# Kernel optimization log

Measured on AMD Instinct MI355X. Metric: run time of the kernel, lower is better.

Reference implementation:

```python
import jax, jax.numpy as jnp
import numpy as np

Bsz, T, D = 2, 2048, 1024
H_ATTN, HD, WIN = 16, 64, 128
H_SSM, DI, N, DCONV, DTR = 8, 2048, 16, 4, 64
P = DI // H_SSM
DT_MIN, DT_MAX = 1e-4, 1.0
EPS = 1e-6


def setup_inputs() -> dict:
    key = jax.random.key(0)
    ks = jax.random.split(key, 16)
    def g(i, shp, s=0.02):
        return jax.random.normal(ks[i], shp, jnp.float32) * s
    TOT = 2 * DI + DTR + 2 * H_SSM * N
    # dt_bias = inverse_softplus(dt) with dt log-uniform in [dt_min, dt_max]
    dt0 = jnp.exp(jax.random.uniform(ks[14], (H_SSM,), jnp.float32) * (np.log(DT_MAX) - np.log(DT_MIN)) + np.log(DT_MIN))
    dt_bias = dt0 + jnp.log(-jnp.expm1(-dt0))
    return dict(
        x=jax.random.normal(ks[0], (Bsz, T, D), jnp.float32),
        norm1_w=jnp.ones((D,), jnp.float32),
        norm2_w=jnp.ones((D,), jnp.float32),
        Win=g(1, (TOT, D)),
        Wdt=g(2, (H_SSM, DTR)),
        conv_w=g(3, (DI, DCONV), 0.2),
        conv_b=jnp.zeros((DI,), jnp.float32),
        A_log=jnp.log(jnp.broadcast_to(jnp.arange(1, N + 1, dtype=jnp.float32), (H_SSM, N))),
        Dskip=jnp.ones((H_SSM, P), jnp.float32),
        dt_bias=dt_bias,
        ssd_norm_w=jnp.ones((DI,), jnp.float32),
        Wout_ssd=g(4, (D, DI)),
        Wres=g(5, (DI, D)),
        Wq=g(6, (D, D)), Wk=g(7, (D, D)), Wv=g(8, (D, D)), Wo=g(9, (D, D)),
    )


def _rms(x, w):
    return x * jax.lax.rsqrt(jnp.mean(x * x, -1, keepdims=True) + EPS) * w


def _silu(x):
    return x * jax.nn.sigmoid(x)


def _dwconv(x, w, b):
    # causal depthwise conv1d: x [B,T,C], w [C,K], left-pad K-1
    K = w.shape[1]
    xp = jnp.pad(x, ((0, 0), (K - 1, 0), (0, 0)))
    y = sum(xp[:, k:k + x.shape[1], :] * w[:, k] for k in range(K))
    return y + b


def _rope(q, k):
    # q,k: [B,H,T,HD]
    inv = 1.0 / (10000.0 ** (jnp.arange(0, HD, 2, dtype=jnp.float32) / HD))
    t = jnp.arange(q.shape[2], dtype=jnp.float32)
    f = jnp.concatenate([t[:, None] * inv, t[:, None] * inv], -1)  # [T,HD]
    cos, sin = jnp.cos(f), jnp.sin(f)
    def rot(x):
        h = x.shape[-1] // 2
        return jnp.concatenate([-x[..., h:], x[..., :h]], -1)
    return q * cos + rot(q) * sin, k * cos + rot(k) * sin


def _ssd_branch(u, Win, Wdt, conv_w, conv_b, A_log, Dskip, dt_bias, ssd_norm_w, Wout_ssd, Wres):
    B = u.shape[0]
    proj = u @ Win.T  # [B,T,4416]
    xin = proj[..., :DI]
    z = proj[..., DI:2 * DI]
    dtl = proj[..., 2 * DI:2 * DI + DTR]
    o = 2 * DI + DTR
    Bm = proj[..., o:o + H_SSM * N].reshape(B, T, H_SSM, N)
    Cm = proj[..., o + H_SSM * N:].reshape(B, T, H_SSM, N)
    xc = _silu(_dwconv(xin, conv_w, conv_b))
    dt = jnp.clip(jax.nn.softplus(dtl @ Wdt.T + dt_bias), DT_MIN, DT_MAX)  # [B,T,H]
    A = -jnp.exp(A_log)  # [H,N]
    xh = xc.reshape(B, T, H_SSM, P)
    dA = jnp.exp(dt[..., None] * A)  # [B,T,H,N]
    dtB = dt[..., None] * Bm        # [B,T,H,N]

    def step(h, inp):
        dA_t, dtB_t, x_t, C_t = inp
        h = h * dA_t[:, :, None, :] + x_t[..., None] * dtB_t[:, :, None, :]
        y = jnp.einsum('bhpn,bhn->bhp', h, C_t)
        return h, y

    h0 = jnp.zeros((B, H_SSM, P, N), u.dtype)
    _, ys = jax.lax.scan(step, h0, (
        dA.transpose(1, 0, 2, 3), dtB.transpose(1, 0, 2, 3),
        xh.transpose(1, 0, 2, 3), Cm.transpose(1, 0, 2, 3)))
    y = ys.transpose(1, 0, 2, 3) + Dskip * xh  # [B,T,H,P]
    y = y.reshape(B, T, DI) + u @ Wres.T       # residual_proj(d_model->d_inner)
    y = _rms(y * _silu(z), ssd_norm_w)         # fused gated RMSNorm
    return y @ Wout_ssd.T


def _attn(u, Wq, Wk, Wv, Wo):
    B = u.shape[0]
    q = (u @ Wq.T).reshape(B, T, H_ATTN, HD).transpose(0, 2, 1, 3)
    k = (u @ Wk.T).reshape(B, T, H_ATTN, HD).transpose(0, 2, 1, 3)
    v = (u @ Wv.T).reshape(B, T, H_ATTN, HD).transpose(0, 2, 1, 3)
    q, k = _rope(q, k)
    s = jnp.einsum('bhtd,bhsd->bhts', q, k) / np.sqrt(HD).astype(np.float32)
    rel = jnp.arange(T)[:, None] - jnp.arange(T)[None, :]
    allowed = (rel >= 0) & (rel < WIN)  # causal sliding window
    s = jnp.where(allowed, s, jnp.float32(-1e30))
    p = jax.nn.softmax(s, axis=-1)
    y = jnp.einsum('bhts,bhsd->bhtd', p, v)
    return y.transpose(0, 2, 1, 3).reshape(B, T, D) @ Wo.T


def reference(x, norm1_w, norm2_w, Win, Wdt, conv_w, conv_b, A_log, Dskip, dt_bias,
              ssd_norm_w, Wout_ssd, Wres, Wq, Wk, Wv, Wo):
    h = x + _ssd_branch(_rms(x, norm1_w), Win, Wdt, conv_w, conv_b, A_log, Dskip,
                        dt_bias, ssd_norm_w, Wout_ssd, Wres)
    return h + _attn(_rms(h, norm2_w), Wq, Wk, Wv, Wo)
```

## Files before the change

kernel.cpp:

```cpp
#include <hip/hip_runtime.h>
#include <stdint.h>

typedef unsigned short u16;
typedef unsigned int u32;
typedef __attribute__((ext_vector_type(8))) short short8;
typedef __attribute__((ext_vector_type(4))) unsigned short ushort4v;
typedef __attribute__((ext_vector_type(4))) float f32x4;

#define Bsz 2
#define Tn 2048
#define Dm 1024
#define H_ATTN 16
#define HDx 64
#define WINx 128
#define H_SSM 8
#define DIx 2048
#define Nst 16
#define DTRx 64
#define Px 256
#define TOTx 4416
#define TOT2 6464
#define RESOFF 4416
#define OFFC (2*DIx+DTRx+H_SSM*Nst)
#define BT (Bsz*Tn)
#define NCH 32
#define LCH 64

__device__ __forceinline__ float b2f(u16 u){ u32 x = ((u32)u)<<16; float f; __builtin_memcpy(&f,&x,4); return f; }
__device__ __forceinline__ u16 f2b(float f){ u32 x; __builtin_memcpy(&x,&f,4); u32 r = x + 0x7fffu + ((x>>16)&1u); return (u16)(r>>16); }

__device__ __forceinline__ float block_sum256(float v){
  #pragma unroll
  for (int o=32;o;o>>=1) v += __shfl_xor(v,o,64);
  __shared__ float sb[4];
  int wid = threadIdx.x>>6;
  if ((threadIdx.x&63)==0) sb[wid]=v;
  __syncthreads();
  v = sb[0]+sb[1]+sb[2]+sb[3];
  __syncthreads();
  return v;
}

__device__ __forceinline__ void gload_lds16(const void* g, void* l){
  __builtin_amdgcn_global_load_lds((const __attribute__((address_space(1))) void*)g,
                                   (__attribute__((address_space(3))) void*)l, 16, 0, 0);
}

struct CvtArgs { const float* s[7]; u16* d[7]; int n[7]; };
__global__ __launch_bounds__(256) void k_cvt_all(CvtArgs a, int total4){
  int i = blockIdx.x*256 + threadIdx.x;
  if (i >= total4) return;
  int e = i*4;
  #pragma unroll
  for (int j=0;j<7;j++){
    if (e < a.n[j]){
      float4 v = *(const float4*)(a.s[j]+e);
      u16* d = a.d[j]+e;
      d[0]=f2b(v.x); d[1]=f2b(v.y); d[2]=f2b(v.z); d[3]=f2b(v.w);
      return;
    }
    e -= a.n[j];
  }
}

__global__ __launch_bounds__(256) void k_rms1024(const float* __restrict__ src, const float* __restrict__ w,
                                                 u16* __restrict__ dst){
  int row = blockIdx.x, tid = threadIdx.x;
  const float* s = src + (size_t)row*1024;
  float v[4]; float ss=0.f;
  #pragma unroll
  for (int i=0;i<4;i++){ v[i] = s[tid + i*256]; ss += v[i]*v[i]; }
  ss = block_sum256(ss);
  float sc = rsqrtf(ss*(1.0f/1024.0f) + 1e-6f);
  u16* d = dst + (size_t)row*1024;
  #pragma unroll
  for (int i=0;i<4;i++){ int c = tid+i*256; d[c] = f2b(v[i]*sc*w[c]); }
}

#define BKq 64

__global__ __launch_bounds__(512,1)
void k_gemm256(const u16* __restrict__ A, const u16* __restrict__ W,
               u16* __restrict__ C16, int M, int N, int K, int gxx){
  __shared__ u16 lds[2][4][128*64];
  int tid = threadIdx.x, lane = tid&63, wid = tid>>6;
  int bid = blockIdx.x;
  int xcd = bid&7, r = bid>>3;
  int halfg = gxx>>1;
  int row0 = (xcd>>1)<<2, col0 = (xcd&1)*halfg;
  int bx = col0 + (r>>2), by = row0 + (r&3);
  int bm = by*256, bn = bx*256;
  int wr = wid>>2, wcn = wid&3;
  int fr = lane&15, fq = lane>>4;
  f32x4 acc[2][2][4][2];
  #pragma unroll
  for (int a=0;a<2;a++)
    #pragma unroll
    for (int b=0;b<2;b++)
      #pragma unroll
      for (int c=0;c<4;c++)
        #pragma unroll
        for (int d=0;d<2;d++)
          #pragma unroll
          for (int rr=0;rr<4;rr++) acc[a][b][c][d][rr]=0.f;

  auto stageHalf = [&](int b, int q, int tt){
    int k0 = tt*BKq;
    #pragma unroll
    for (int i=0;i<2;i++){
      int idx = i*512 + tid;
      int row = idx>>3, c8 = idx&7;
      const u16* src; int gr;
      if (q < 2){ gr = bm + q*128 + row;     if (gr > M-1) gr = M-1; src = A; }
      else      { gr = bn + (q-2)*128 + row; if (gr > N-1) gr = N-1; src = W; }
      gload_lds16(src + (size_t)gr*K + k0 + ((c8 ^ (row&7)))*8, &lds[b][q][(size_t)idx*8]);
    }
  };
  auto loadA = [&](const u16* aP, short8 (&af)[2][4]){
    #pragma unroll
    for (int kk=0;kk<2;kk++)
      #pragma unroll
      for (int mi=0;mi<4;mi++){
        int row = wr*64 + mi*16 + fr;
        af[kk][mi] = *(const short8*)(aP + row*64 + ((kk*4+fq) ^ (row&7))*8);
      }
  };
  auto loadB = [&](const u16* bP, short8 (&bf)[2][2]){
    #pragma unroll
    for (int kk=0;kk<2;kk++)
      #pragma unroll
      for (int ni=0;ni<2;ni++){
        int row = wcn*32 + ni*16 + fr;
        bf[kk][ni] = *(const short8*)(bP + row*64 + ((kk*4+fq) ^ (row&7))*8);
      }
  };

  int NT = K/BKq;
  stageHalf(0,0,0); stageHalf(0,2,0); stageHalf(0,3,0); stageHalf(0,1,0);

  short8 af[2][4], bf0[2][2], bf1[2][2];
  for (int t=0;t<NT;t++){
    int cb = t&1, nb = cb^1;
    int tn = (t+1 < NT) ? t+1 : t;
    const u16* A0 = &lds[cb][0][0];
    const u16* A1 = &lds[cb][1][0];
    const u16* B0 = &lds[cb][2][0];
    const u16* B1 = &lds[cb][3][0];
    stageHalf(nb,0,tn);
    asm volatile("s_waitcnt vmcnt(6)" ::: "memory");
    __builtin_amdgcn_sched_barrier(0);
    __builtin_amdgcn_s_barrier();
    loadA(A0, af); loadB(B0, bf0);
    asm volatile("s_waitcnt lgkmcnt(0)" ::: "memory");
    __builtin_amdgcn_sched_barrier(0);
    __builtin_amdgcn_s_setprio(1);
    #pragma unroll
    for (int kk=0;kk<2;kk++)
      #pragma unroll
      for (int mi=0;mi<4;mi++)
        #pragma unroll
        for (int ni=0;ni<2;ni++)
          acc[0][0][mi][ni] = __builtin_amdgcn_mfma_f32_16x16x32_bf16(af[kk][mi], bf0[kk][ni], acc[0][0][mi][ni], 0,0,0);
    __builtin_amdgcn_s_setprio(0);
    __builtin_amdgcn_s_barrier();
    stageHalf(nb,2,tn);
    asm volatile("s_waitcnt vmcnt(6)" ::: "memory");
    __builtin_amdgcn_sched_barrier(0);
    __builtin_amdgcn_s_barrier();
    loadB(B1, bf1);
    asm volatile("s_waitcnt lgkmcnt(0)" ::: "memory");
    __builtin_amdgcn_sched_barrier(0);
    __builtin_amdgcn_s_setprio(1);
    #pragma unroll
    for (int kk=0;kk<2;kk++)
      #pragma unroll
      for (int mi=0;mi<4;mi++)
        #pragma unroll
        for (int ni=0;ni<2;ni++)
          acc[0][1][mi][ni] = __builtin_amdgcn_mfma_f32_16x16x32_bf16(af[kk][mi], bf1[kk][ni], acc[0][1][mi][ni], 0,0,0);
    __builtin_amdgcn_s_setprio(0);
    __builtin_amdgcn_s_barrier();
    stageHalf(nb,3,tn);
    asm volatile("s_waitcnt vmcnt(6)" ::: "memory");
    __builtin_amdgcn_sched_barrier(0);
    __builtin_amdgcn_s_barrier();
    loadA(A1, af);
    asm volatile("s_waitcnt lgkmcnt(0)" ::: "memory");
    __builtin_amdgcn_sched_barrier(0);
    __builtin_amdgcn_s_setprio(1);
    #pragma unroll
    for (int kk=0;kk<2;kk++)
      #pragma unroll
      for (int mi=0;mi<4;mi++)
        #pragma unroll
        for (int ni=0;ni<2;ni++)
          acc[1][1][mi][ni] = __builtin_amdgcn_mfma_f32_16x16x32_bf16(af[kk][mi], bf1[kk][ni], acc[1][1][mi][ni], 0,0,0);
    __builtin_amdgcn_s_setprio(0);
    __builtin_amdgcn_s_barrier();
    stageHalf(nb,1,tn);
    asm volatile("s_waitcnt vmcnt(6)" ::: "memory");
    __builtin_amdgcn_sched_barrier(0);
    __builtin_amdgcn_s_barrier();
    __builtin_amdgcn_s_setprio(1);
    #pragma unroll
    for (int kk=0;kk<2;kk++)
      #pragma unroll
      for (int mi=0;mi<4;mi++)
        #pragma unroll
        for (int ni=0;ni<2;ni++)
          acc[1][0][mi][ni] = __builtin_amdgcn_mfma_f32_16x16x32_bf16(af[kk][mi], bf0[kk][ni], acc[1][0][mi][ni], 0,0,0);
    __builtin_amdgcn_s_setprio(0);
    __builtin_amdgcn_s_barrier();
  }
  #pragma unroll
  for (int mh=0;mh<2;mh++)
    #pragma unroll
    for (int nh=0;nh<2;nh++)
      #pragma unroll
      for (int mi=0;mi<4;mi++)
        #pragma unroll
        for (int ni=0;ni<2;ni++){
          int row0o = bm + mh*128 + wr*64 + mi*16 + fq*4;
          int col  = bn + nh*128 + wcn*32 + ni*16 + fr;
          if (col < N){
            #pragma unroll
            for (int rr=0;rr<4;rr++)
              C16[(size_t)(row0o+rr)*N + col] = f2b(acc[mh][nh][mi][ni][rr]);
          }
        }
}

template<int NWC>
__global__ __launch_bounds__(256, (NWC==2?2:3))
void k_gemm(const u16* __restrict__ A, const u16* __restrict__ W,
            float* __restrict__ C, u16* __restrict__ C16, const float* __restrict__ ADD,
            int M, int N, int K, int gx, int mode){
  constexpr int BN    = 64*NWC;
  constexpr int ROWS  = 128 + BN;
  constexpr int NLOADS= ROWS/32;
  constexpr int MFRAG = (NWC==2)?4:2;
  __shared__ u16 lds[2][ROWS*64];
  int tid = threadIdx.x, lane = tid&63, wid = tid>>6;
  int nwg = gridDim.x;
  int cpx = nwg>>3;
  int bid = blockIdx.x;
  int swz = (bid&7)*cpx + (bid>>3);
  int fourgx = gx<<2;
  int super = swz / fourgx;
  int r     = swz % fourgx;
  int bx = r >> 2;
  int by = (super<<2) + (r&3);
  int bm = by*128, bn = bx*BN;
  int wc = (NWC==2) ? (wid&1) : 0;
  int wr = (NWC==2) ? (wid>>1) : wid;
  int fr = lane&15, fq = lane>>4;
  int s7 = fr&7;
  f32x4 acc[MFRAG][4];
  #pragma unroll
  for (int mi=0;mi<MFRAG;mi++)
    #pragma unroll
    for (int ni=0;ni<4;ni++)
      #pragma unroll
      for (int rr=0;rr<4;rr++) acc[mi][ni][rr]=0.f;

  auto stage = [&](int buf, int t){
    int k0 = t*BKq;
    #pragma unroll
    for (int i=0;i<NLOADS;i++){
      int chunk = i*256 + tid;
      int row = chunk>>3, c8 = chunk&7;
      const u16* src;
      if (row < 128){ int ra = bm + row; if (ra > M-1) ra = M-1; src = A + (size_t)ra*K; }
      else          { int rb = bn + row-128; if (rb > N-1) rb = N-1; src = W + (size_t)rb*K; }
      gload_lds16(src + k0 + ((c8 ^ (row&7)))*8, &lds[buf][(size_t)chunk*8]);
    }
  };

  int NT = K/BKq;
  stage(0, 0);
  stage(1, 1);
  for (int t=0;t<NT;t++){
    int cur = t&1;
    if (t+1 < NT){
      if constexpr (NWC==2) asm volatile("s_waitcnt vmcnt(8)" ::: "memory");
      else                  asm volatile("s_waitcnt vmcnt(6)" ::: "memory");
    } else {
      asm volatile("s_waitcnt vmcnt(0)" ::: "memory");
    }
    __builtin_amdgcn_sched_barrier(0);
    __builtin_amdgcn_s_barrier();
    #pragma unroll
    for (int kk=0;kk<2;kk++){
      short8 bf4[4], af4[MFRAG];
      int slotb = ((kk*4 + fq) ^ s7)*8;
      #pragma unroll
      for (int ni=0;ni<4;ni++)
        bf4[ni] = *(const short8*)(&lds[cur][(128 + wc*64 + ni*16 + fr)*64 + slotb]);
      #pragma unroll
      for (int mi=0;mi<MFRAG;mi++)
        af4[mi] = *(const short8*)(&lds[cur][(wr*(MFRAG*16) + mi*16 + fr)*64 + slotb]);
      #pragma unroll
      for (int mi=0;mi<MFRAG;mi++)
        #pragma unroll
        for (int ni=0;ni<4;ni++)
          acc[mi][ni] = __builtin_amdgcn_mfma_f32_16x16x32_bf16(af4[mi], bf4[ni], acc[mi][ni], 0,0,0);
    }
    asm volatile("s_waitcnt lgkmcnt(0)" ::: "memory");
    __builtin_amdgcn_sched_barrier(0);
    __builtin_amdgcn_s_barrier();
    if (t+2 < NT) stage(cur, t+2);
  }
  #pragma unroll
  for (int mi=0;mi<MFRAG;mi++){
    int row0 = bm + wr*(MFRAG*16) + mi*16 + fq*4;
    #pragma unroll
    for (int ni=0;ni<4;ni++){
      int col = bn + wc*64 + ni*16 + fr;
      if (col < N){
        #pragma unroll
        for (int rr=0;rr<4;rr++){
          size_t idx = (size_t)(row0+rr)*N + col;
          float v = acc[mi][ni][rr];
          if (mode == 0)      C[idx] = v;
          else if (mode == 2) C16[idx] = f2b(v);
          else                C[idx] = ADD[idx] + v;
        }
      }
    }
  }
}

__global__ __launch_bounds__(256) void k_dtprep(const u16* __restrict__ proj, const float* __restrict__ Wdt,
      const float* __restrict__ dt_bias, const float* __restrict__ A_log,
      float* __restrict__ dtA, float* __restrict__ dtB){
  int idx = blockIdx.x*256 + threadIdx.x;
  int h = idx & 7; int bt = idx >> 3;
  const u16* dtl  = proj + (size_t)bt*TOT2 + 2*DIx;
  const float* wrow = Wdt + h*64;
  float v = dt_bias[h];
  #pragma unroll
  for (int i8=0;i8<8;i8++){
    short8 dv = *(const short8*)(dtl + i8*8);
    #pragma unroll
    for (int e=0;e<8;e++) v += b2f((u16)dv[e])*wrow[i8*8+e];
  }
  float sp = (v > 20.0f) ? v : log1pf(expf(v));
  float dt = fminf(fmaxf(sp, 1e-4f), 1.0f);
  const u16* bm = proj + (size_t)bt*TOT2 + 2*DIx + DTRx + h*16;
  short8 b0 = *(const short8*)(bm);
  short8 b1 = *(const short8*)(bm+8);
  #pragma unroll
  for (int n=0;n<16;n++){
    float Av = -expf(A_log[h*16+n]);
    float bv = (n<8) ? b2f((u16)b0[n]) : b2f((u16)b1[n-8]);
    dtA[(size_t)idx*16+n] = dt*Av;
    dtB[(size_t)idx*16+n] = dt*bv;
  }
}

__global__ __launch_bounds__(256) void k_scan1(const float* __restrict__ dtA, const float* __restrict__ dtB,
    const u16* __restrict__ proj, const float* __restrict__ cw, const float* __restrict__ cb,
    float* __restrict__ expS, u16* __restrict__ y, float* __restrict__ LS){
  __shared__ float sA[1024], sS[1024], sB[1024], sC[1024];
  int bx = blockIdx.x;
  int c = bx & 31, h = (bx>>5)&7, b = bx>>8;
  int tid = threadIdx.x;
  size_t t0 = (size_t)b*Tn + c*64;
  int j = tid>>2, n0 = (tid&3)*4;
  {
    size_t ga = (t0 + j)*128 + h*16 + n0;
    float4 va = *(const float4*)(dtA + ga);
    float4 vb = *(const float4*)(dtB + ga);
    ushort4v vc = *(const ushort4v*)(proj + (t0 + j)*TOT2 + OFFC + h*16 + n0);
    *(float4*)(&sA[j*16+n0]) = va;
    *(float4*)(&sB[j*16+n0]) = vb;
    sC[j*16+n0+0] = b2f(vc[0]); sC[j*16+n0+1] = b2f(vc[1]);
    sC[j*16+n0+2] = b2f(vc[2]); sC[j*16+n0+3] = b2f(vc[3]);
  }
  __syncthreads();
  if (tid < 16){
    float cum = 0.f;
    for (int jj=0;jj<64;jj++){ cum += sA[jj*16+tid]; sS[jj*16+tid] = cum; }
  }
  __syncthreads();
  {
    float e[4], s4[4];
    #pragma unroll
    for (int i=0;i<4;i++){ e[i] = expf(sA[j*16+n0+i]); s4[i] = expf(sS[j*16+n0+i]); }
    #pragma unroll
    for (int i=0;i<4;i++){ sA[j*16+n0+i] = e[i]; sS[j*16+n0+i] = s4[i]; }
    float4 ev; ev.x=s4[0]; ev.y=s4[1]; ev.z=s4[2]; ev.w=s4[3];
    *(float4*)(expS + (t0+j)*128 + h*16 + n0) = ev;
  }
  __syncthreads();
  float st[16];
  #pragma unroll
  for (int n=0;n<16;n++) st[n]=0.f;
  int ch = h*Px + tid;
  const u16* pxin = proj + t0*TOT2 + ch;
  const u16* pres = proj + t0*TOT2 + RESOFF + ch;
  float w0=cw[ch*4+0], w1=cw[ch*4+1], w2=cw[ch*4+2], w3=cw[ch*4+3];
  float bcv = cb[ch];
  float x3=0.f, x2=0.f, x1=0.f;
  if (c > 0){
    x3 = b2f(pxin[-(ptrdiff_t)3*TOT2]);
    x2 = b2f(pxin[-(ptrdiff_t)2*TOT2]);
    x1 = b2f(pxin[-(ptrdiff_t)TOT2]);
  }
  u16* yp = y + t0*DIx + ch;
  for (int jj=0;jj<64;jj++){
    float x0 = b2f(pxin[(size_t)jj*TOT2]);
    float cv = bcv + x3*w0 + x2*w1 + x1*w2 + x0*w3;
    float x = cv / (1.0f + expf(-cv));
    x3=x2; x2=x1; x1=x0;
    float acc = b2f(pres[(size_t)jj*TOT2]);
    #pragma unroll
    for (int n=0;n<16;n++){ st[n] = st[n]*sA[jj*16+n] + x*sB[jj*16+n]; acc += st[n]*sC[jj*16+n]; }
    yp[(size_t)jj*DIx] = f2b(acc);
  }
  float* ls = LS + ((((size_t)b*8+h)*NCH + c)*Px + tid)*16;
  #pragma unroll
  for (int n=0;n<16;n++) ls[n] = st[n];
}

__global__ __launch_bounds__(256) void k_scan2(const float* __restrict__ expS, const float* __restrict__ LS,
                                               float* __restrict__ H0){
  int bh = blockIdx.x; int b = bh>>3, h = bh&7;
  int tid = threadIdx.x;
  __shared__ float dl[16];
  float Hs[16];
  #pragma unroll
  for (int n=0;n<16;n++) Hs[n]=0.f;
  for (int c=0;c<NCH;c++){
    if (tid<16) dl[tid] = expS[((size_t)b*Tn + c*64 + 63)*128 + h*16 + tid];
    __syncthreads();
    size_t base = ((((size_t)b*8+h)*NCH + c)*Px + tid)*16;
    #pragma unroll
    for (int n=0;n<16;n++){ H0[base+n] = Hs[n]; Hs[n] = Hs[n]*dl[n] + LS[base+n]; }
    __syncthreads();
  }
}

__global__ __launch_bounds__(256) void k_scan3(const u16* __restrict__ proj, const float* __restrict__ expS,
    const float* __restrict__ H0, const float* __restrict__ cw, const float* __restrict__ cb,
    const float* __restrict__ Dskip, u16* __restrict__ y){
  __shared__ float ce[1024];
  int bx = blockIdx.x; int c = bx&31, h=(bx>>5)&7, b=bx>>8;
  int tid = threadIdx.x;
  size_t t0 = (size_t)b*Tn + c*64;
  int j = tid>>2, n0=(tid&3)*4;
  {
    ushort4v cv = *(const ushort4v*)(proj + (t0+j)*TOT2 + OFFC + h*16 + n0);
    float4 evv = *(const float4*)(expS + (t0+j)*128 + h*16 + n0);
    ce[j*16+n0+0] = b2f(cv[0])*evv.x; ce[j*16+n0+1] = b2f(cv[1])*evv.y;
    ce[j*16+n0+2] = b2f(cv[2])*evv.z; ce[j*16+n0+3] = b2f(cv[3])*evv.w;
  }
  __syncthreads();
  float h0[16];
  size_t base = ((((size_t)b*8+h)*NCH + c)*Px + tid)*16;
  #pragma unroll
  for (int n=0;n<16;n++) h0[n] = H0[base+n];
  int ch = h*Px + tid;
  float dsk = Dskip[ch];
  const u16* pxin = proj + t0*TOT2 + ch;
  float w0=cw[ch*4+0], w1=cw[ch*4+1], w2=cw[ch*4+2], w3=cw[ch*4+3];
  float bcv = cb[ch];
  float x3=0.f, x2=0.f, x1=0.f;
  if (c > 0){
    x3 = b2f(pxin[-(ptrdiff_t)3*TOT2]);
    x2 = b2f(pxin[-(ptrdiff_t)2*TOT2]);
    x1 = b2f(pxin[-(ptrdiff_t)TOT2]);
  }
  u16* yp = y + t0*DIx + ch;
  for (int jj=0;jj<64;jj++){
    float x0 = b2f(pxin[(size_t)jj*TOT2]);
    float cv = bcv + x3*w0 + x2*w1 + x1*w2 + x0*w3;
    float x = cv / (1.0f + expf(-cv));
    x3=x2; x2=x1; x1=x0;
    float f = 0.f;
    #pragma unroll
    for (int n=0;n<16;n++) f += ce[jj*16+n]*h0[n];
    size_t yi = (size_t)jj*DIx;
    yp[yi] = f2b(b2f(yp[yi]) + f + dsk*x);
  }
}

__global__ __launch_bounds__(256) void k_gatedrms(const u16* __restrict__ y, const u16* __restrict__ proj,
     const float* __restrict__ w, u16* __restrict__ yn){
  int row = blockIdx.x, tid = threadIdx.x;
  const u16* yr = y + (size_t)row*DIx;
  const u16* zr = proj + (size_t)row*TOT2 + DIx;
  float v[8]; float ss=0.f;
  #pragma unroll
  for (int i=0;i<8;i++){
    int cidx = tid + i*256;
    float z = b2f(zr[cidx]);
    float g = b2f(yr[cidx]) * (z / (1.0f + expf(-z)));
    v[i]=g; ss += g*g;
  }
  ss = block_sum256(ss);
  float sc = rsqrtf(ss*(1.0f/2048.0f) + 1e-6f);
  u16* d = yn + (size_t)row*DIx;
  #pragma unroll
  for (int i=0;i<8;i++){ int cidx=tid+i*256; d[cidx] = f2b(v[i]*sc*w[cidx]); }
}

__global__ __launch_bounds__(256) void k_addrms(const float* __restrict__ x, const float* __restrict__ sout,
     const float* __restrict__ w, float* __restrict__ hbuf, u16* __restrict__ u2){
  int row=blockIdx.x, tid=threadIdx.x;
  float v[4]; float ss=0.f;
  #pragma unroll
  for (int i=0;i<4;i++){
    int cidx = tid + i*256;
    size_t idx = (size_t)row*1024 + cidx;
    float hv = x[idx] + sout[idx];
    hbuf[idx]=hv; v[i]=hv; ss+=hv*hv;
  }
  ss = block_sum256(ss);
  float sc = rsqrtf(ss*(1.0f/1024.0f)+1e-6f);
  #pragma unroll
  for (int i=0;i<4;i++){ int cidx=tid+i*256; u2[(size_t)row*1024+cidx] = f2b(v[i]*sc*w[cidx]); }
}

__global__ __launch_bounds__(256) void k_rope(const u16* __restrict__ qkvb,
    u16* __restrict__ qr, u16* __restrict__ kr, u16* __restrict__ vr){
  int idx = blockIdx.x*256 + threadIdx.x;
  int d = idx & 63;
  int h = (idx>>6) & 15;
  int t = (idx>>10) & 2047;
  int b = idx >> 21;
  int col = idx & 1023;
  size_t base = (size_t)(idx>>10)*3072;
  int dh = d & 31;
  float ang = (float)t * exp2f(-(float)dh * (13.287712379549449f/32.0f));
  float cs = cosf(ang), sn = sinf(ang);
  int part = (d<32) ? 32 : -32;
  float q = b2f(qkvb[base + col]),        qp = b2f(qkvb[base + col + part]);
  float k = b2f(qkvb[base + 1024 + col]), kp = b2f(qkvb[base + 1024 + col + part]);
  float vv = b2f(qkvb[base + 2048 + col]);
  float rq = (d<32)? -qp : qp;
  float rk = (d<32)? -kp : kp;
  size_t dst = (((size_t)b*H_ATTN + h)*Tn + t)*64 + d;
  qr[dst] = f2b(q*cs + rq*sn);
  kr[dst] = f2b(k*cs + rk*sn);
  vr[dst] = f2b(vv);
}

#define QT 64
#define KSPAN 192
__device__ __forceinline__ u32 swz128a(int row, int b){
  return (u32)((row*128 + b) ^ ((((row&7)^((row>>3)&7)))<<4));
}
__device__ __forceinline__ u32 swz384a(int row, int b){
  return (u32)((row*384 + b) ^ ((((row&7)^((row>>3)&7)))<<4));
}

__global__ __launch_bounds__(256) void k_attn_mfma(const u16* __restrict__ qr, const u16* __restrict__ kr,
    const u16* __restrict__ vr, u16* __restrict__ ya){
  __shared__ u16 bufK[KSPAN*64];
  __shared__ u16 bufV[64*KSPAN];
  int tid = threadIdx.x, lane = tid&63, wid = tid>>6;
  int fr = lane&15, fq = lane>>4;
  int blk = blockIdx.x;
  int qt = blk & 31, bh = blk >> 5;
  int t0 = qt*QT;
  size_t rowbase = (size_t)bh*Tn;
  char* cK = (char*)bufK;
  char* cV = (char*)bufV;

  #pragma unroll
  for (int it=0; it<6; ++it){
    int chunk = it*256 + tid;
    int row = chunk>>3, c8 = chunk&7;
    int sg = t0 - 128 + row;
    if (sg >= 0){
      short8 v = *(const short8*)(kr + (rowbase+sg)*64 + c8*8);
      *(short8*)(cK + swz128a(row, c8*16)) = v;
    }
  }
  #pragma unroll
  for (int it=0; it<6; ++it){
    int idx = it*256 + tid;
    int s = idx>>3, c8 = idx&7, d0 = c8*8;
    int sg = t0 - 128 + s;
    short8 v;
    if (sg >= 0) v = *(const short8*)(vr + (rowbase+sg)*64 + d0);
    else         v = short8{0,0,0,0,0,0,0,0};
    #pragma unroll
    for (int e=0;e<8;e++)
      *(u16*)(cV + swz384a(d0+e, s*2)) = (u16)v[e];
  }
  __syncthreads();

  f32x4 acc[12];
  #pragma unroll
  for (int j=0;j<12;j++)
    #pragma unroll
    for (int r=0;r<4;r++) acc[j][r]=0.f;
  #pragma unroll
  for (int kk=0;kk<2;kk++){
    short8 aq = *(const short8*)(qr + (rowbase + t0 + wid*16 + fr)*64 + kk*32 + fq*8);
    #pragma unroll
    for (int j=0;j<12;j++){
      short8 bk = *(const short8*)(cK + swz128a(j*16+fr, kk*64 + fq*16));
      acc[j] = __builtin_amdgcn_mfma_f32_16x16x32_bf16(aq, bk, acc[j], 0,0,0);
    }
  }

  float p[12][4];
  int cb = lane&15;
  #pragma unroll
  for (int r=0;r<4;r++){
    int rq = wid*16 + (lane>>4)*4 + r;
    float m = -3.0e38f;
    #pragma unroll
    for (int j=0;j<12;j++){
      int c = j*16 + cb;
      bool allowed = (c > rq) && (c <= rq+128) && (c >= 128 - t0);
      float v = allowed ? acc[j][r]*0.125f : -3.0e38f;
      p[j][r] = v;
      m = fmaxf(m, v);
    }
    #pragma unroll
    for (int o=1;o<16;o<<=1) m = fmaxf(m, __shfl_xor(m, o, 64));
    float sum = 0.f;
    #pragma unroll
    for (int j=0;j<12;j++){ float e = __expf(p[j][r]-m); p[j][r]=e; sum += e; }
    #pragma unroll
    for (int o=1;o<16;o<<=1) sum += __shfl_xor(sum, o, 64);
    float inv = 1.0f/sum;
    #pragma unroll
    for (int j=0;j<12;j++) p[j][r] *= inv;
  }
  __syncthreads();

  #pragma unroll
  for (int r=0;r<4;r++){
    int rq = wid*16 + (lane>>4)*4 + r;
    #pragma unroll
    for (int j=0;j<12;j++){
      *(u16*)(cK + swz384a(rq, (j*16+cb)*2)) = f2b(p[j][r]);
    }
  }
  __syncthreads();

  f32x4 acc2[4];
  #pragma unroll
  for (int f=0;f<4;f++)
    #pragma unroll
    for (int r=0;r<4;r++) acc2[f][r]=0.f;
  #pragma unroll
  for (int kk=0;kk<6;kk++){
    short8 ap = *(const short8*)(cK + swz384a(wid*16 + fr, kk*64 + fq*16));
    #pragma unroll
    for (int f=0;f<4;f++){
      short8 bv = *(const short8*)(cV + swz384a(f*16+fr, kk*64 + fq*16));
      acc2[f] = __builtin_amdgcn_mfma_f32_16x16x32_bf16(ap, bv, acc2[f], 0,0,0);
    }
  }
  int b = bh >> 4, h = bh & 15;
  #pragma unroll
  for (int f=0;f<4;f++){
    int d = f*16 + cb;
    #pragma unroll
    for (int r=0;r<4;r++){
      int q = t0 + wid*16 + (lane>>4)*4 + r;
      ya[((size_t)b*Tn + q)*Dm + h*64 + d] = f2b(acc2[f][r]);
    }
  }
}

extern "C" void kernel_launch(void* const* d_in, const int* in_sizes, int n_in,
                              void* d_out, int out_size, void* d_ws, size_t ws_size,
                              hipStream_t stream) {
  const float* x        = (const float*)d_in[0];
  const float* norm1_w  = (const float*)d_in[1];
  const float* norm2_w  = (const float*)d_in[2];
  const float* Win      = (const float*)d_in[3];
  const float* Wdt      = (const float*)d_in[4];
  const float* conv_w   = (const float*)d_in[5];
  const float* conv_b   = (const float*)d_in[6];
  const float* A_log    = (const float*)d_in[7];
  const float* Dskip    = (const float*)d_in[8];
  const float* dt_bias  = (const float*)d_in[9];
  const float* ssd_norm = (const float*)d_in[10];
  const float* Wout_ssd = (const float*)d_in[11];
  const float* Wres     = (const float*)d_in[12];
  const float* Wq       = (const float*)d_in[13];
  const float* Wk       = (const float*)d_in[14];
  const float* Wv       = (const float*)d_in[15];
  const float* Wo       = (const float*)d_in[16];

  char* ws = (char*)d_ws;
  size_t off = 0;
  auto alloc = [&](size_t bytes){ size_t r = off; off += (bytes + 255) & ~(size_t)255; return r; };

  size_t o_WinB  = alloc((size_t)TOTx*Dm*2);
  size_t o_WresB = alloc((size_t)DIx*Dm*2);
  size_t o_WoutB = alloc((size_t)Dm*DIx*2);
  size_t o_WqB   = alloc((size_t)Dm*Dm*2);
  size_t o_WkB   = alloc((size_t)Dm*Dm*2);
  size_t o_WvB   = alloc((size_t)Dm*Dm*2);
  size_t o_WoB   = alloc((size_t)Dm*Dm*2);
  size_t o_u1    = alloc((size_t)BT*Dm*2);
  size_t o_proj  = alloc((size_t)BT*TOT2*2);
  size_t o_sout  = alloc((size_t)BT*Dm*4);
  size_t o_dtA   = alloc((size_t)BT*H_SSM*Nst*4);
  size_t o_dtB   = alloc((size_t)BT*H_SSM*Nst*4);
  size_t o_expS  = alloc((size_t)BT*H_SSM*Nst*4);
  size_t o_LS    = alloc((size_t)Bsz*H_SSM*NCH*Px*Nst*4);
  size_t o_H0    = alloc((size_t)Bsz*H_SSM*NCH*Px*Nst*4);
  size_t o_y     = alloc((size_t)BT*DIx*2);
  size_t o_yn    = alloc((size_t)BT*DIx*2);
  size_t o_hb    = alloc((size_t)BT*Dm*4);
  size_t o_qr    = alloc((size_t)Bsz*H_ATTN*Tn*HDx*2);
  size_t o_kr    = alloc((size_t)Bsz*H_ATTN*Tn*HDx*2);

  u16* WinB  = (u16*)(ws + o_WinB);
  u16* WoutB = (u16*)(ws + o_WoutB);
  u16* WqB   = (u16*)(ws + o_WqB);
  u16* u1    = (u16*)(ws + o_u1);
  u16* projb = (u16*)(ws + o_proj);
  float* dtA  = (float*)(ws + o_dtA);
  float* dtB  = (float*)(ws + o_dtB);
  float* expS = (float*)(ws + o_expS);
  float* LS   = (float*)(ws + o_LS);
  float* H0   = (float*)(ws + o_H0);
  u16*   ybuf16 = (u16*)(ws + o_y);
  u16*   yn   = (u16*)(ws + o_yn);
  float* hb   = (float*)(ws + o_hb);
  float* sout = (float*)(ws + o_sout);
  u16* qkvb = (u16*)(ws + o_proj);
  u16* qr = (u16*)(ws + o_qr);
  u16* kr = (u16*)(ws + o_kr);
  u16* vr = u1;
  u16* yatt = (u16*)(ws + o_y);

  {
    CvtArgs a;
    a.s[0]=Win;  a.d[0]=WinB;  a.n[0]=TOTx*Dm;
    a.s[1]=Wres; a.d[1]=(u16*)(ws + o_WresB); a.n[1]=DIx*Dm;
    a.s[2]=Wout_ssd; a.d[2]=WoutB; a.n[2]=Dm*DIx;
    a.s[3]=Wq; a.d[3]=WqB; a.n[3]=Dm*Dm;
    a.s[4]=Wk; a.d[4]=(u16*)(ws + o_WkB); a.n[4]=Dm*Dm;
    a.s[5]=Wv; a.d[5]=(u16*)(ws + o_WvB); a.n[5]=Dm*Dm;
    a.s[6]=Wo; a.d[6]=(u16*)(ws + o_WoB); a.n[6]=Dm*Dm;
    int total4 = (a.n[0]+a.n[1]+a.n[2]+a.n[3]+a.n[4]+a.n[5]+a.n[6])/4;
    k_cvt_all<<<dim3((total4+255)/256), dim3(256), 0, stream>>>(a, total4);
  }

  k_rms1024<<<dim3(BT), dim3(256), 0, stream>>>(x, norm1_w, u1);
  k_gemm256<<<dim3(16*26), dim3(512), 0, stream>>>(u1, WinB, projb, BT, TOT2, Dm, 26);
  k_dtprep<<<dim3(BT*H_SSM/256), dim3(256), 0, stream>>>(projb, Wdt, dt_bias, A_log, dtA, dtB);
  k_scan1<<<dim3(Bsz*H_SSM*NCH), dim3(256), 0, stream>>>(dtA, dtB, projb, conv_w, conv_b, expS, ybuf16, LS);
  k_scan2<<<dim3(Bsz*H_SSM), dim3(256), 0, stream>>>(expS, LS, H0);
  k_scan3<<<dim3(Bsz*H_SSM*NCH), dim3(256), 0, stream>>>(projb, expS, H0, conv_w, conv_b, Dskip, ybuf16);
  k_gatedrms<<<dim3(BT), dim3(256), 0, stream>>>(ybuf16, projb, ssd_norm, yn);
  k_gemm<1><<<dim3(16*32), dim3(256), 0, stream>>>(yn, WoutB, sout, nullptr, nullptr, BT, Dm, DIx, 16, 0);
  k_addrms<<<dim3(BT), dim3(256), 0, stream>>>(x, sout, norm2_w, hb, (u16*)(ws + o_yn));
  u16* u2p = (u16*)(ws + o_yn);
  k_gemm<1><<<dim3(48*32), dim3(256), 0, stream>>>(u2p, WqB, nullptr, qkvb, nullptr, BT, 3*Dm, Dm, 48, 2);
  k_rope<<<dim3(BT*Dm/256), dim3(256), 0, stream>>>(qkvb, qr, kr, vr);
  k_attn_mfma<<<dim3(Bsz*H_ATTN*(Tn/QT)), dim3(256), 0, stream>>>(qr, kr, vr, yatt);
  k_gemm<1><<<dim3(16*32), dim3(256), 0, stream>>>(yatt, (u16*)(ws + o_WoB), (float*)d_out, nullptr, hb, BT, Dm, Dm, 16, 3);
  (void)in_sizes; (void)n_in; (void)out_size; (void)ws_size;
}
```

Baseline: 337.0 us.

## Collapse four-phase GEMM pipeline into one staged tile per iteration

Replaces the four-quadrant interleaved prefetch/compute schedule, which had a barrier and LDS wait per quadrant, with a simpler loop. Each iteration issues all four global→LDS stages for the next tile, waits for the current tile, loads all A/B fragments from LDS, then runs all four quadrant MFMA blocks back to back. This cuts barriers per k-step from eight to two. In exchange it holds more fragment registers at once (af0 and af1), which may raise register pressure and lower occupancy, and it loses the fine-grained overlap of LDS reads with MFMA.

```diff
diff --git a/kernel.cpp b/kernel.cpp
--- a/kernel.cpp
+++ b/kernel.cpp
@@ -136,80 +136,58 @@
   };
 
   int NT = K/BKq;
-  stageHalf(0,0,0); stageHalf(0,2,0); stageHalf(0,3,0); stageHalf(0,1,0);
-
-  short8 af[2][4], bf0[2][2], bf1[2][2];
+  stageHalf(0,0,0); stageHalf(0,1,0); stageHalf(0,2,0); stageHalf(0,3,0);
+
   for (int t=0;t<NT;t++){
     int cb = t&1, nb = cb^1;
-    int tn = (t+1 < NT) ? t+1 : t;
-    const u16* A0 = &lds[cb][0][0];
-    const u16* A1 = &lds[cb][1][0];
-    const u16* B0 = &lds[cb][2][0];
-    const u16* B1 = &lds[cb][3][0];
-    stageHalf(nb,0,tn);
-    asm volatile("s_waitcnt vmcnt(6)" ::: "memory");
+    if (t+1 < NT){
+      stageHalf(nb,0,t+1); stageHalf(nb,1,t+1); stageHalf(nb,2,t+1); stageHalf(nb,3,t+1);
+      asm volatile("s_waitcnt vmcnt(8)" ::: "memory");
+    } else {
+      asm volatile("s_waitcnt vmcnt(0)" ::: "memory");
+    }
     __builtin_amdgcn_sched_barrier(0);
     __builtin_amdgcn_s_barrier();
-    loadA(A0, af); loadB(B0, bf0);
-    asm volatile("s_waitcnt lgkmcnt(0)" ::: "memory");
     __builtin_amdgcn_sched_barrier(0);
-    __builtin_amdgcn_s_setprio(1);
-    #pragma unroll
-    for (int kk=0;kk<2;kk++)
-      #pragma unroll
-      for (int mi=0;mi<4;mi++)
+    {
+      const u16* A0 = &lds[cb][0][0];
+      const u16* A1 = &lds[cb][1][0];
+      const u16* B0 = &lds[cb][2][0];
+      const u16* B1 = &lds[cb][3][0];
+      short8 af0[2][4], af1[2][4], bf0[2][2], bf1[2][2];
+      loadA(A0, af0); loadB(B0, bf0); loadB(B1, bf1); loadA(A1, af1);
+      __builtin_amdgcn_s_setprio(1);
+      #pragma unroll
+      for (int kk=0;kk<2;kk++)
         #pragma unroll
-        for (int ni=0;ni<2;ni++)
-          acc[0][0][mi][ni] = __builtin_amdgcn_mfma_f32_16x16x32_bf16(af[kk][mi], bf0[kk][ni], acc[0][0][mi][ni], 0,0,0);
-    __builtin_amdgcn_s_setprio(0);
-    __builtin_amdgcn_s_barrier();
-    stageHalf(nb,2,tn);
-    asm volatile("s_waitcnt vmcnt(6)" ::: "memory");
+        for (int mi=0;mi<4;mi++)
+          #pragma unroll
+          for (int ni=0;ni<2;ni++)
+            acc[0][0][mi][ni] = __builtin_amdgcn_mfma_f32_16x16x32_bf16(af0[kk][mi], bf0[kk][ni], acc[0][0][mi][ni], 0,0,0);
+      #pragma unroll
+      for (int kk=0;kk<2;kk++)
+        #pragma unroll
+        for (int mi=0;mi<4;mi++)
+          #pragma unroll
+          for (int ni=0;ni<2;ni++)
+            acc[0][1][mi][ni] = __builtin_amdgcn_mfma_f32_16x16x32_bf16(af0[kk][mi], bf1[kk][ni], acc[0][1][mi][ni], 0,0,0);
+      #pragma unroll
+      for (int kk=0;kk<2;kk++)
+        #pragma unroll
+        for (int mi=0;mi<4;mi++)
+          #pragma unroll
+          for (int ni=0;ni<2;ni++)
+            acc[1][1][mi][ni] = __builtin_amdgcn_mfma_f32_16x16x32_bf16(af1[kk][mi], bf1[kk][ni], acc[1][1][mi][ni], 0,0,0);
+      #pragma unroll
+      for (int kk=0;kk<2;kk++)
+        #pragma unroll
+        for (int mi=0;mi<4;mi++)
+          #pragma unroll
+          for (int ni=0;ni<2;ni++)
+            acc[1][0][mi][ni] = __builtin_amdgcn_mfma_f32_16x16x32_bf16(af1[kk][mi], bf0[kk][ni], acc[1][0][mi][ni], 0,0,0);
+      __builtin_amdgcn_s_setprio(0);
+    }
     __builtin_amdgcn_sched_barrier(0);
-    __builtin_amdgcn_s_barrier();
-    loadB(B1, bf1);
-    asm volatile("s_waitcnt lgkmcnt(0)" ::: "memory");
-    __builtin_amdgcn_sched_barrier(0);
-    __builtin_amdgcn_s_setprio(1);
-    #pragma unroll
-    for (int kk=0;kk<2;kk++)
-      #pragma unroll
-      for (int mi=0;mi<4;mi++)
-        #pragma unroll
-        for (int ni=0;ni<2;ni++)
-          acc[0][1][mi][ni] = __builtin_amdgcn_mfma_f32_16x16x32_bf16(af[kk][mi], bf1[kk][ni], acc[0][1][mi][ni], 0,0,0);
-    __builtin_amdgcn_s_setprio(0);
-    __builtin_amdgcn_s_barrier();
-    stageHalf(nb,3,tn);
-    asm volatile("s_waitcnt vmcnt(6)" ::: "memory");
-    __builtin_amdgcn_sched_barrier(0);
-    __builtin_amdgcn_s_barrier();
-    loadA(A1, af);
-    asm volatile("s_waitcnt lgkmcnt(0)" ::: "memory");
-    __builtin_amdgcn_sched_barrier(0);
-    __builtin_amdgcn_s_setprio(1);
-    #pragma unroll
-    for (int kk=0;kk<2;kk++)
-      #pragma unroll
-      for (int mi=0;mi<4;mi++)
-        #pragma unroll
-        for (int ni=0;ni<2;ni++)
-          acc[1][1][mi][ni] = __builtin_amdgcn_mfma_f32_16x16x32_bf16(af[kk][mi], bf1[kk][ni], acc[1][1][mi][ni], 0,0,0);
-    __builtin_amdgcn_s_setprio(0);
-    __builtin_amdgcn_s_barrier();
-    stageHalf(nb,1,tn);
-    asm volatile("s_waitcnt vmcnt(6)" ::: "memory");
-    __builtin_amdgcn_sched_barrier(0);
-    __builtin_amdgcn_s_barrier();
-    __builtin_amdgcn_s_setprio(1);
-    #pragma unroll
-    for (int kk=0;kk<2;kk++)
-      #pragma unroll
-      for (int mi=0;mi<4;mi++)
-        #pragma unroll
-        for (int ni=0;ni<2;ni++)
-          acc[1][0][mi][ni] = __builtin_amdgcn_mfma_f32_16x16x32_bf16(af[kk][mi], bf0[kk][ni], acc[1][0][mi][ni], 0,0,0);
-    __builtin_amdgcn_s_setprio(0);
     __builtin_amdgcn_s_barrier();
   }
   #pragma unroll
```

Result: no change. 341.0 us (+1.2%).

## Fuse RoPE and head-layout scatter into QKV GEMM epilogue; parallelize scan2

Applied to the files above, without the earlier changes.

The QKV projection GEMM now has an epilogue mode that applies rotary embedding in registers and writes q, k, v directly in [B,H,T,64] layout. This drops the separate rope kernel and the round trip of the bf16 qkv intermediate through memory. Separately, the inter-chunk state scan is spread over 16x more blocks, with one thread per (channel, state) pair instead of one block per (batch, head), which removes the shared-memory broadcast and barriers. The GEMM epilogue writes become scattered 2-byte stores, and each thread now computes sin/cos in the epilogue.

```diff
diff --git a/kernel.cpp b/kernel.cpp
--- a/kernel.cpp
+++ b/kernel.cpp
@@ -234,6 +234,7 @@
 __global__ __launch_bounds__(256, (NWC==2?2:3))
 void k_gemm(const u16* __restrict__ A, const u16* __restrict__ W,
             float* __restrict__ C, u16* __restrict__ C16, const float* __restrict__ ADD,
+            u16* __restrict__ qro, u16* __restrict__ kro, u16* __restrict__ vro,
             int M, int N, int K, int gx, int mode){
   constexpr int BN    = 64*NWC;
   constexpr int ROWS  = 128 + BN;
@@ -310,6 +311,36 @@
     __builtin_amdgcn_s_barrier();
     if (t+2 < NT) stage(cur, t+2);
   }
+  if (mode == 5){
+    int sec = bn >> 10;
+    int hh  = (bn >> 6) & 15;
+    #pragma unroll
+    for (int mi=0;mi<MFRAG;mi++){
+      #pragma unroll
+      for (int rr=0;rr<4;rr++){
+        int row = bm + wr*(MFRAG*16) + mi*16 + fq*4 + rr;
+        int tt = row & (Tn-1), bb = row >> 11;
+        size_t dstb = (((size_t)bb*H_ATTN + hh)*Tn + tt)*64;
+        if (sec == 2){
+          #pragma unroll
+          for (int ni=0;ni<4;ni++)
+            vro[dstb + ni*16 + fr] = f2b(acc[mi][ni][rr]);
+        } else {
+          u16* dst = (sec==0) ? qro : kro;
+          #pragma unroll
+          for (int ni=0;ni<2;ni++){
+            int dh = ni*16 + fr;
+            float ang = (float)tt * exp2f(-(float)dh * (13.287712379549449f/32.0f));
+            float cs = cosf(ang), sn = sinf(ang);
+            float lo = acc[mi][ni][rr], hi = acc[mi][ni+2][rr];
+            dst[dstb + dh]      = f2b(lo*cs - hi*sn);
+            dst[dstb + dh + 32] = f2b(hi*cs + lo*sn);
+          }
+        }
+      }
+    }
+    return;
+  }
   #pragma unroll
   for (int mi=0;mi<MFRAG;mi++){
     int row0 = bm + wr*(MFRAG*16) + mi*16 + fq*4;
@@ -425,19 +456,18 @@
 
 __global__ __launch_bounds__(256) void k_scan2(const float* __restrict__ expS, const float* __restrict__ LS,
                                                float* __restrict__ H0){
-  int bh = blockIdx.x; int b = bh>>3, h = bh&7;
+  int blk = blockIdx.x;
+  int slice = blk & 15;
+  int bh = blk >> 4; int b = bh>>3, h = bh&7;
   int tid = threadIdx.x;
-  __shared__ float dl[16];
-  float Hs[16];
-  #pragma unroll
-  for (int n=0;n<16;n++) Hs[n]=0.f;
+  int ch = slice*16 + (tid>>4);
+  int n  = tid & 15;
+  float Hs = 0.f;
   for (int c=0;c<NCH;c++){
-    if (tid<16) dl[tid] = expS[((size_t)b*Tn + c*64 + 63)*128 + h*16 + tid];
-    __syncthreads();
-    size_t base = ((((size_t)b*8+h)*NCH + c)*Px + tid)*16;
-    #pragma unroll
-    for (int n=0;n<16;n++){ H0[base+n] = Hs[n]; Hs[n] = Hs[n]*dl[n] + LS[base+n]; }
-    __syncthreads();
+    float dl = expS[((size_t)b*Tn + c*64 + 63)*128 + h*16 + n];
+    size_t base = ((((size_t)b*8+h)*NCH + c)*Px + ch)*16 + n;
+    H0[base] = Hs;
+    Hs = Hs*dl + LS[base];
   }
 }
 
@@ -520,30 +550,6 @@
   float sc = rsqrtf(ss*(1.0f/1024.0f)+1e-6f);
   #pragma unroll
   for (int i=0;i<4;i++){ int cidx=tid+i*256; u2[(size_t)row*1024+cidx] = f2b(v[i]*sc*w[cidx]); }
-}
-
-__global__ __launch_bounds__(256) void k_rope(const u16* __restrict__ qkvb,
-    u16* __restrict__ qr, u16* __restrict__ kr, u16* __restrict__ vr){
-  int idx = blockIdx.x*256 + threadIdx.x;
-  int d = idx & 63;
-  int h = (idx>>6) & 15;
-  int t = (idx>>10) & 2047;
-  int b = idx >> 21;
-  int col = idx & 1023;
-  size_t base = (size_t)(idx>>10)*3072;
-  int dh = d & 31;
-  float ang = (float)t * exp2f(-(float)dh * (13.287712379549449f/32.0f));
-  float cs = cosf(ang), sn = sinf(ang);
-  int part = (d<32) ? 32 : -32;
-  float q = b2f(qkvb[base + col]),        qp = b2f(qkvb[base + col + part]);
-  float k = b2f(qkvb[base + 1024 + col]), kp = b2f(qkvb[base + 1024 + col + part]);
-  float vv = b2f(qkvb[base + 2048 + col]);
-  float rq = (d<32)? -qp : qp;
-  float rk = (d<32)? -kp : kp;
-  size_t dst = (((size_t)b*H_ATTN + h)*Tn + t)*64 + d;
-  qr[dst] = f2b(q*cs + rq*sn);
-  kr[dst] = f2b(k*cs + rk*sn);
-  vr[dst] = f2b(vv);
 }
 
 #define QT 64
@@ -730,7 +736,6 @@
   u16*   yn   = (u16*)(ws + o_yn);
   float* hb   = (float*)(ws + o_hb);
   float* sout = (float*)(ws + o_sout);
-  u16* qkvb = (u16*)(ws + o_proj);
   u16* qr = (u16*)(ws + o_qr);
   u16* kr = (u16*)(ws + o_kr);
   u16* vr = u1;
@@ -753,15 +758,17 @@
   k_gemm256<<<dim3(16*26), dim3(512), 0, stream>>>(u1, WinB, projb, BT, TOT2, Dm, 26);
   k_dtprep<<<dim3(BT*H_SSM/256), dim3(256), 0, stream>>>(projb, Wdt, dt_bias, A_log, dtA, dtB);
   k_scan1<<<dim3(Bsz*H_SSM*NCH), dim3(256), 0, stream>>>(dtA, dtB, projb, conv_w, conv_b, expS, ybuf16, LS);
-  k_scan2<<<dim3(Bsz*H_SSM), dim3(256), 0, stream>>>(expS, LS, H0);
+  k_scan2<<<dim3(Bsz*H_SSM*16), dim3(256), 0, stream>>>(expS, LS, H0);
   k_scan3<<<dim3(Bsz*H_SSM*NCH), dim3(256), 0, stream>>>(projb, expS, H0, conv_w, conv_b, Dskip, ybuf16);
   k_gatedrms<<<dim3(BT), dim3(256), 0, stream>>>(ybuf16, projb, ssd_norm, yn);
-  k_gemm<1><<<dim3(16*32), dim3(256), 0, stream>>>(yn, WoutB, sout, nullptr, nullptr, BT, Dm, DIx, 16, 0);
+  k_gemm<1><<<dim3(16*32), dim3(256), 0, stream>>>(yn, WoutB, sout, nullptr, nullptr,
+                                                   nullptr, nullptr, nullptr, BT, Dm, DIx, 16, 0);
   k_addrms<<<dim3(BT), dim3(256), 0, stream>>>(x, sout, norm2_w, hb, (u16*)(ws + o_yn));
   u16* u2p = (u16*)(ws + o_yn);
-  k_gemm<1><<<dim3(48*32), dim3(256), 0, stream>>>(u2p, WqB, nullptr, qkvb, nullptr, BT, 3*Dm, Dm, 48, 2);
-  k_rope<<<dim3(BT*Dm/256), dim3(256), 0, stream>>>(qkvb, qr, kr, vr);
+  k_gemm<1><<<dim3(48*32), dim3(256), 0, stream>>>(u2p, WqB, nullptr, nullptr, nullptr,
+                                                   qr, kr, vr, BT, 3*Dm, Dm, 48, 5);
   k_attn_mfma<<<dim3(Bsz*H_ATTN*(Tn/QT)), dim3(256), 0, stream>>>(qr, kr, vr, yatt);
-  k_gemm<1><<<dim3(16*32), dim3(256), 0, stream>>>(yatt, (u16*)(ws + o_WoB), (float*)d_out, nullptr, hb, BT, Dm, Dm, 16, 3);
+  k_gemm<1><<<dim3(16*32), dim3(256), 0, stream>>>(yatt, (u16*)(ws + o_WoB), (float*)d_out, nullptr, hb,
+                                                   nullptr, nullptr, nullptr, BT, Dm, Dm, 16, 3);
   (void)in_sizes; (void)n_in; (void)out_size; (void)ws_size;
 }
```

New measurement: 321.0 us. 1.05x faster.
